# Kernel optimization log

Hardware: AMD Instinct MI355X
Metric: run time of the kernel (lower is better)

Reference implementation:

```python
import jax, jax.numpy as jnp
from jax import lax
import numpy as np

N = 2000      # num_nodes
T_IN = 24
T_OUT = 12
B = 32
H = 64        # hidden_dim
D = 10        # embed_dim / adapt_dim
K = 2         # cheb_k
C_IN = 1


def setup_inputs() -> dict:
    key = jax.random.key(0)
    ks = jax.random.split(key, 13)
    s = 0.1  # xavier-ish scale
    f32 = jnp.float32
    return {
        "x": jax.random.normal(ks[0], (B, T_IN, N), f32),
        "node_emb": jax.random.normal(ks[1], (N, D), f32) * s,
        "adapt_emb": jax.random.normal(ks[2], (N, D), f32) * s,
        # layer 0 NAPL weight/bias pools (gate: 2H out, candidate: H out)
        "Wg0": jax.random.normal(ks[3], (D, K, C_IN + H, 2 * H), f32) * s,
        "bg0": jax.random.normal(ks[4], (D, 2 * H), f32) * s,
        "Wc0": jax.random.normal(ks[5], (D, K, C_IN + H, H), f32) * s,
        "bc0": jax.random.normal(ks[6], (D, H), f32) * s,
        # layer 1 pools (input is hidden_dim)
        "Wg1": jax.random.normal(ks[7], (D, K, 2 * H, 2 * H), f32) * s,
        "bg1": jax.random.normal(ks[8], (D, 2 * H), f32) * s,
        "Wc1": jax.random.normal(ks[9], (D, K, 2 * H, H), f32) * s,
        "bc1": jax.random.normal(ks[10], (D, H), f32) * s,
        # 1x1 conv head == per-node linear hidden -> T_out
        "head_w": jax.random.normal(ks[11], (T_OUT, H), f32) * s,
        "head_b": jnp.zeros((T_OUT,), f32),
    }


def reference(x, node_emb, adapt_emb, Wg0, bg0, Wc0, bc0, Wg1, bg1, Wc1, bc1,
              head_w, head_b):
    Bn, T, Nn = x.shape
    # adaptive adjacency: row-softmax(relu(E E^T)); no prior -> A_used = A_adapt
    A = jax.nn.softmax(jax.nn.relu(adapt_emb @ adapt_emb.T), axis=-1)
    supports = jnp.stack([jnp.eye(Nn, dtype=x.dtype), A])  # (K, N, N)

    def napl(Wp, bp):
        # node-adaptive parameter learning: per-node weights/biases
        W = jnp.einsum('nd,dkio->nkio', node_emb, Wp)  # (N, K, Cin, Cout)
        b = node_emb @ bp                              # (N, Cout)
        return W, b

    p = [napl(Wg0, bg0), napl(Wc0, bc0), napl(Wg1, bg1), napl(Wc1, bc1)]

    def gconv(inp, W, b):
        # inp: (B, N, C)
        xg = jnp.einsum('knm,bmc->bknc', supports, inp)      # (B, K, N, C)
        return jnp.einsum('bkni,nkio->bno', xg, W) + b       # (B, N, Cout)

    def cell(xt, h, gW, gb, cW, cb):
        zr = jax.nn.sigmoid(gconv(jnp.concatenate([xt, h], -1), gW, gb))
        z, r = jnp.split(zr, 2, axis=-1)
        hc = jnp.tanh(gconv(jnp.concatenate([xt, r * h], -1), cW, cb))
        return z * h + (1.0 - z) * hc

    def step(carry, xt):
        h0, h1 = carry
        h0 = cell(xt, h0, p[0][0], p[0][1], p[1][0], p[1][1])
        h1 = cell(h0, h1, p[2][0], p[2][1], p[3][0], p[3][1])
        return (h0, h1), None

    xs = jnp.transpose(x[..., None], (1, 0, 2, 3))  # (T, B, N, 1)
    h0 = jnp.zeros((Bn, Nn, H), x.dtype)
    h1 = jnp.zeros((Bn, Nn, H), x.dtype)
    (h0, h1), _ = lax.scan(step, (h0, h1), xs)

    # 1x1 conv head on (B, H, N, 1) == per-node linear: (B, T_out, N)
    y = jnp.einsum('bnh,oh->bon', h1, head_w) + head_b[None, :, None]
    return y
```

## Files before the change

kernel.cpp:

```cpp
#include <hip/hip_runtime.h>
#include <math.h>

#define NN 2000
#define BB 32
#define TT 24
#define T_OUT 12
#define HH 64
#define DD 10
#define NP 2048
#define BC 2048

typedef unsigned short ushort_t;
typedef __bf16 bf16x8 __attribute__((ext_vector_type(8)));
typedef float f32x4 __attribute__((ext_vector_type(4)));

__device__ __forceinline__ float sigmoidf_(float x) { return 1.f / (1.f + expf(-x)); }

__device__ __forceinline__ ushort_t f2bf(float f) {
    unsigned int u = __float_as_uint(f);
    unsigned int r = (u + 0x7FFFu + ((u >> 16) & 1u)) >> 16;
    return (ushort_t)r;
}
__device__ __forceinline__ float bf2f(ushort_t s) {
    return __uint_as_float(((unsigned int)s) << 16);
}

__device__ __forceinline__ void glld16(const ushort_t* g, ushort_t* lds) {
    __builtin_amdgcn_global_load_lds(
        (const __attribute__((address_space(1))) char*)g,
        (__attribute__((address_space(3))) char*)lds, 16, 0, 0);
}

__device__ __forceinline__ unsigned lds_off(const void* p) {
    return (unsigned)(size_t)(__attribute__((address_space(3))) const char*)p;
}

constexpr size_t SZ_NPNP2 = (size_t)NP * NP * 2;
constexpr size_t SZ_ST4   = (size_t)NN * BC * 4;
constexpr size_t SZ_NPB2  = (size_t)NP * BC * 2;

constexpr size_t ABF_OFF  = 0;
constexpr size_t H0F_OFF  = ABF_OFF + SZ_NPNP2;
constexpr size_t H1F_OFF  = H0F_OFF + SZ_ST4;
constexpr size_t ZF_OFF   = H1F_OFF + SZ_ST4;
constexpr size_t H0B_OFF  = ZF_OFF + SZ_ST4;
constexpr size_t H1B_OFF  = H0B_OFF + SZ_NPB2;
constexpr size_t RHB_OFF  = H1B_OFF + SZ_NPB2;
constexpr size_t AH0_OFF  = RHB_OFF + SZ_NPB2;
constexpr size_t AHX_OFF  = AH0_OFF + SZ_NPB2;
constexpr size_t AXF_OFF  = AHX_OFF + SZ_NPB2;
constexpr size_t BTG0_OFF = AXF_OFF + (size_t)BB * TT * NN * 4;
constexpr size_t BTC0_OFF = BTG0_OFF + (size_t)DD * 128 * 128 * 2;
constexpr size_t BTG1_OFF = BTC0_OFF + (size_t)DD * 64 * 128 * 2;
constexpr size_t BTC1_OFF = BTG1_OFF + (size_t)DD * 128 * 256 * 2;
constexpr size_t WS_TOP   = BTC1_OFF + (size_t)DD * 64 * 256 * 2;
constexpr size_t ZF1_OFF  = WS_TOP;
constexpr size_t RHB1_OFF = ZF1_OFF + SZ_ST4;
constexpr size_t AHY_OFF  = RHB1_OFF + SZ_NPB2;
constexpr size_t TOP_PIPE = AHY_OFF + SZ_NPB2;

__global__ __launch_bounds__(256) void compute_A_kernel(const float* __restrict__ E,
                                                        float* __restrict__ A) {
    const int row = blockIdx.x;
    const int tid = threadIdx.x;
    float er[DD];
#pragma unroll
    for (int d = 0; d < DD; ++d) er[d] = E[row * DD + d];
    __shared__ float red[8];

    float lmax = -1e30f;
    for (int c = tid; c < NN; c += 256) {
        float s = 0.f;
#pragma unroll
        for (int d = 0; d < DD; ++d) s += er[d] * E[c * DD + d];
        s = fmaxf(s, 0.f);
        A[(size_t)row * NN + c] = s;
        lmax = fmaxf(lmax, s);
    }
#pragma unroll
    for (int o = 32; o > 0; o >>= 1) lmax = fmaxf(lmax, __shfl_down(lmax, o, 64));
    if ((tid & 63) == 0) red[tid >> 6] = lmax;
    __syncthreads();
    const float rmax = fmaxf(fmaxf(red[0], red[1]), fmaxf(red[2], red[3]));
    __syncthreads();

    float lsum = 0.f;
    for (int c = tid; c < NN; c += 256) {
        float v = expf(A[(size_t)row * NN + c] - rmax);
        A[(size_t)row * NN + c] = v;
        lsum += v;
    }
#pragma unroll
    for (int o = 32; o > 0; o >>= 1) lsum += __shfl_down(lsum, o, 64);
    if ((tid & 63) == 0) red[4 + (tid >> 6)] = lsum;
    __syncthreads();
    const float inv = 1.f / (red[4] + red[5] + red[6] + red[7]);
    for (int c = tid; c < NN; c += 256) A[(size_t)row * NN + c] *= inv;
}

__global__ __launch_bounds__(256) void convert_A(const float* __restrict__ Af,
                                                 ushort_t* __restrict__ Ab) {
    size_t idx = (size_t)blockIdx.x * 256 + threadIdx.x;
    int r = (int)(idx >> 11), c = (int)(idx & 2047);
    float v = (r < NN && c < NN) ? Af[(size_t)r * NN + c] : 0.f;
    Ab[idx] = f2bf(v);
}

__global__ __launch_bounds__(256) void ax2_kernel(const float* __restrict__ A,
                                                  const float* __restrict__ x,
                                                  float* __restrict__ Ax) {
    __shared__ float As[64][66];
    __shared__ float xs[64][50];
    const int n0 = blockIdx.x * 64;
    const int b0 = blockIdx.y * 2;
    const int tid = threadIdx.x;
    const int tr = tid >> 4, tc = tid & 15;
    float acc[4][3] = {};

    for (int m0 = 0; m0 < NN; m0 += 64) {
#pragma unroll
        for (int l = 0; l < 16; ++l) {
            int idx = tid + l * 256;
            int mm = idx & 63, r = idx >> 6;
            int n = n0 + r, m = m0 + mm;
            As[mm][r] = (n < NN && m < NN) ? A[(size_t)n * NN + m] : 0.f;
        }
#pragma unroll
        for (int l = 0; l < 12; ++l) {
            int idx = tid + l * 256;
            int mm = idx & 63, col = idx >> 6;
            int m = m0 + mm;
            int bl = col / 24, t = col - bl * 24;
            xs[mm][col] = (m < NN) ? x[((size_t)(b0 + bl) * TT + t) * NN + m] : 0.f;
        }
        __syncthreads();
#pragma unroll 4
        for (int mm = 0; mm < 64; ++mm) {
            float2 a01 = *(const float2*)&As[mm][tr * 4];
            float2 a23 = *(const float2*)&As[mm][tr * 4 + 2];
            float xv[3];
            xv[0] = xs[mm][tc * 3];
            xv[1] = xs[mm][tc * 3 + 1];
            xv[2] = xs[mm][tc * 3 + 2];
            float av[4] = {a01.x, a01.y, a23.x, a23.y};
#pragma unroll
            for (int i = 0; i < 4; ++i)
#pragma unroll
                for (int j = 0; j < 3; ++j) acc[i][j] += av[i] * xv[j];
        }
        __syncthreads();
    }
#pragma unroll
    for (int i = 0; i < 4; ++i) {
        const int n = n0 + tr * 4 + i;
        if (n < NN) {
#pragma unroll
            for (int j = 0; j < 3; ++j) {
                int col = tc * 3 + j;
                int bl = col / 24, t = col - bl * 24;
                Ax[((size_t)(b0 + bl) * TT + t) * NN + n] = acc[i][j];
            }
        }
    }
}


__device__ __forceinline__ void gemm_body(int bx, int by,
                                          const ushort_t* __restrict__ Ab,
                                          const ushort_t* __restrict__ H,
                                          ushort_t* __restrict__ Y, char* smem) {
    ushort_t* As = (ushort_t*)smem;
    ushort_t* Bs = (ushort_t*)(smem + 8192);
    const int tid = threadIdx.x;
    const int w = tid >> 6, l = tid & 63, lr = l & 15, lg = l >> 4;
    const int n0 = bx * 64, j0 = by * 128;
    f32x4 acc[4][2] = {};

    const unsigned bs0 = lds_off(Bs);
    const unsigned btr_b[2] = {
        bs0 + 2u * ((unsigned)(w * 2 + 0) * 512 + (unsigned)lg * 128 + (unsigned)lr),
        bs0 + 2u * ((unsigned)(w * 2 + 1) * 512 + (unsigned)lg * 128 + (unsigned)lr)};

    for (int ks = 0; ks < NP / 64; ++ks) {
        const int k0 = ks * 64;
#pragma unroll
        for (int p = 0; p < 2; ++p) {
            const int idx = p * 256 + tid;
            const int row = idx >> 3, sl = idx & 7;
            glld16(Ab + (size_t)(n0 + row) * NP + k0 + ((sl ^ (row & 7)) << 3),
                   (ushort_t*)((char*)As + idx * 16));
        }
#pragma unroll
        for (int p = 0; p < 4; ++p) {
            const int idx = p * 256 + tid;
            const int g = idx >> 9, li = idx & 511;
            const int row = k0 + g * 32 + ((li >> 3) & 7) * 4 + ((li >> 1) & 3);
            const int col = j0 + (li >> 6) * 16 + (li & 1) * 8;
            glld16(H + (size_t)row * BC + col,
                   (ushort_t*)((char*)Bs + g * 8192 + li * 16));
        }
        __syncthreads();

        bf16x8 av[2][4];
#pragma unroll
        for (int kk = 0; kk < 2; ++kk)
#pragma unroll
            for (int m = 0; m < 4; ++m) {
                const int rr = m * 16 + lr;
                av[kk][m] = *(const bf16x8*)&As[rr * 64 + (((kk * 4 + lg) ^ (rr & 7)) << 3)];
            }
        unsigned long long bq[2][2][2];
        asm volatile(
            "ds_read_b64_tr_b16 %0, %8 offset:0\n\t"
            "ds_read_b64_tr_b16 %1, %8 offset:128\n\t"
            "ds_read_b64_tr_b16 %2, %9 offset:0\n\t"
            "ds_read_b64_tr_b16 %3, %9 offset:128\n\t"
            "ds_read_b64_tr_b16 %4, %8 offset:8192\n\t"
            "ds_read_b64_tr_b16 %5, %8 offset:8320\n\t"
            "ds_read_b64_tr_b16 %6, %9 offset:8192\n\t"
            "ds_read_b64_tr_b16 %7, %9 offset:8320"
            : "=v"(bq[0][0][0]), "=v"(bq[0][0][1]), "=v"(bq[0][1][0]), "=v"(bq[0][1][1]),
              "=v"(bq[1][0][0]), "=v"(bq[1][0][1]), "=v"(bq[1][1][0]), "=v"(bq[1][1][1])
            : "v"(btr_b[0]), "v"(btr_b[1]));
        asm volatile("s_waitcnt lgkmcnt(0)" ::: "memory");
        __builtin_amdgcn_sched_barrier(0);
        bf16x8 bv[2][2];
#pragma unroll
        for (int kk = 0; kk < 2; ++kk)
#pragma unroll
            for (int nt = 0; nt < 2; ++nt) {
                union { unsigned long long q[2]; bf16x8 f; } u;
                u.q[0] = bq[kk][nt][0];
                u.q[1] = bq[kk][nt][1];
                bv[kk][nt] = u.f;
            }

#pragma unroll
        for (int kk = 0; kk < 2; ++kk)
#pragma unroll
            for (int m = 0; m < 4; ++m)
#pragma unroll
                for (int nt = 0; nt < 2; ++nt)
                    acc[m][nt] = __builtin_amdgcn_mfma_f32_16x16x32_bf16(av[kk][m], bv[kk][nt], acc[m][nt], 0, 0, 0);
        __syncthreads();
    }

#pragma unroll
    for (int m = 0; m < 4; ++m)
#pragma unroll
        for (int r = 0; r < 4; ++r) {
            const int n = n0 + m * 16 + lg * 4 + r;
            if (n < NN) {
#pragma unroll
                for (int nt = 0; nt < 2; ++nt)
                    Y[(size_t)n * BC + j0 + w * 32 + nt * 16 + lr] = f2bf(acc[m][nt][r]);
            }
        }
}

template <int NSEGS, int CO, bool GATE, bool HASX>
__device__ __forceinline__ void napl_body(
    int bid, char* smem,
    const ushort_t* __restrict__ Bt, const float* __restrict__ bp,
    const float* __restrict__ emb, const float* __restrict__ WxPool,
    const ushort_t* __restrict__ s0p, const ushort_t* __restrict__ s1p,
    const ushort_t* __restrict__ s2p, const ushort_t* __restrict__ s3p,
    const float* __restrict__ xv, const float* __restrict__ axv,
    const float* hf, float* __restrict__ zf,
    ushort_t* __restrict__ outb, float* outf, int t) {
    constexpr int K = NSEGS * 64;
    constexpr int NT = (CO == 128) ? 2 : 1;
    constexpr int NHALF = NSEGS / 2;
    ushort_t* As = (ushort_t*)smem;
    const int tid = threadIdx.x;
    const int w = tid >> 6, l = tid & 63, lr = l & 15, lg = l >> 4;
    const int n0 = bid * 2;
    const int ob = w * (16 * NT);
    const ushort_t* segs[4] = {s0p, s1p, s2p, s3p};

#pragma unroll
    for (int s = 0; s < NSEGS; ++s) {
        const ushort_t* sp = segs[s];
#pragma unroll
        for (int p = 0; p < 2; ++p) {
            const int idx = p * 256 + tid;
            const int row = idx >> 3, c16 = idx & 7;
            glld16(sp + (size_t)(n0 + (row >> 5)) * BC + (row & 31) * 64 +
                       ((c16 ^ (row & 7)) << 3),
                   (ushort_t*)((char*)As + s * 8192 + idx * 16));
        }
    }
    __syncthreads();

    f32x4 OUT[4][NT] = {};
#pragma unroll 1
    for (int hf2 = 0; hf2 < NHALF; ++hf2) {
        bf16x8 av[4][4];
#pragma unroll
        for (int c = 0; c < 4; ++c) {
            const int s = hf2 * 2 + (c >> 1);
            const int kin = (c & 1) * 32 + lg * 8;
#pragma unroll
            for (int m = 0; m < 4; ++m) {
                const int rr = m * 16 + lr;
                av[c][m] = *(const bf16x8*)&As[s * 4096 + rr * 64 + (kin ^ ((rr & 7) << 3))];
            }
        }
#pragma unroll 1
        for (int d = 0; d < DD; ++d) {
            const ushort_t* btd = Bt + (size_t)d * CO * K;
            const float ea = emb[n0 * DD + d];
            const float eb = emb[(n0 + 1) * DD + d];
            f32x4 P[4][NT] = {};
#pragma unroll
            for (int c = 0; c < 4; ++c) {
                const int kg = (hf2 * 2 + (c >> 1)) * 64 + (c & 1) * 32 + lg * 8;
                bf16x8 bv[NT];
#pragma unroll
                for (int nt = 0; nt < NT; ++nt)
                    bv[nt] = *(const bf16x8*)&btd[(size_t)(ob + nt * 16 + lr) * K + kg];
#pragma unroll
                for (int m = 0; m < 4; ++m)
#pragma unroll
                    for (int nt = 0; nt < NT; ++nt)
                        P[m][nt] = __builtin_amdgcn_mfma_f32_16x16x32_bf16(av[c][m], bv[nt], P[m][nt], 0, 0, 0);
            }
#pragma unroll
            for (int m = 0; m < 4; ++m) {
                const float e = (m < 2) ? ea : eb;
#pragma unroll
                for (int nt = 0; nt < NT; ++nt)
#pragma unroll
                    for (int r = 0; r < 4; ++r)
                        OUT[m][nt][r] += e * P[m][nt][r];
            }
        }
    }

    float bias[2][NT];
#pragma unroll
    for (int nd = 0; nd < 2; ++nd)
#pragma unroll
        for (int nt = 0; nt < NT; ++nt) {
            float s_ = 0.f;
#pragma unroll
            for (int d = 0; d < DD; ++d)
                s_ += emb[(n0 + nd) * DD + d] * bp[d * CO + ob + nt * 16 + lr];
            bias[nd][nt] = s_;
        }
    float wx[2][2][NT] = {};
    if (HASX) {
#pragma unroll
        for (int kk = 0; kk < 2; ++kk)
#pragma unroll
            for (int nd = 0; nd < 2; ++nd)
#pragma unroll
                for (int nt = 0; nt < NT; ++nt) {
                    float s_ = 0.f;
#pragma unroll
                    for (int d = 0; d < DD; ++d)
                        s_ += emb[(n0 + nd) * DD + d] *
                              WxPool[(size_t)(d * 2 + kk) * 65 * CO + ob + nt * 16 + lr];
                    wx[kk][nd][nt] = s_;
                }
    }

#pragma unroll
    for (int m = 0; m < 4; ++m) {
        const int nd = m >> 1;
        const int n = n0 + nd;
#pragma unroll
        for (int r = 0; r < 4; ++r) {
            const int row = m * 16 + lg * 4 + r;
            const int b = row & 31;
            const size_t nb = (size_t)n * BC + b * 64;
            float xt = 0.f, axt = 0.f;
            if (HASX) {
                xt = xv[((size_t)b * TT + t) * NN + n];
                axt = axv[((size_t)b * TT + t) * NN + n];
            }
#pragma unroll
            for (int nt = 0; nt < NT; ++nt) {
                const int o = ob + nt * 16 + lr;
                float val = OUT[m][nt][r] + bias[nd][nt];
                if (HASX) val += xt * wx[0][nd][nt] + axt * wx[1][nd][nt];
                if (GATE) {
                    const float sg = sigmoidf_(val);
                    if (ob < 64) {
                        zf[nb + o] = sg;
                    } else {
                        outb[nb + (o - 64)] = f2bf(sg * hf[nb + (o - 64)]);
                    }
                } else {
                    const float hc = tanhf(val);
                    const float z = zf[nb + o];
                    const float hn = z * hf[nb + o] + (1.f - z) * hc;
                    outf[nb + o] = hn;
                    outb[nb + o] = f2bf(hn);
                }
            }
        }
    }
}


__global__ __launch_bounds__(256) void gemm_trb(const ushort_t* __restrict__ Ab,
                                                const ushort_t* __restrict__ H0,
                                                ushort_t* __restrict__ Y0,
                                                const ushort_t* __restrict__ H1,
                                                ushort_t* __restrict__ Y1) {
    __shared__ __align__(16) char smem[24576];
    gemm_body(blockIdx.x, blockIdx.y, Ab,
              (blockIdx.z == 0) ? H0 : H1, (blockIdx.z == 0) ? Y0 : Y1, smem);
}

template <int NSEGS, int CO, bool GATE, bool HASX>
__global__ __launch_bounds__(256) void napl2(
    const ushort_t* __restrict__ Bt, const float* __restrict__ bp,
    const float* __restrict__ emb, const float* __restrict__ WxPool,
    const ushort_t* __restrict__ s0p, const ushort_t* __restrict__ s1p,
    const ushort_t* __restrict__ s2p, const ushort_t* __restrict__ s3p,
    const float* __restrict__ xv, const float* __restrict__ axv,
    const float* hf, float* __restrict__ zf,
    ushort_t* __restrict__ outb, float* outf, int t) {
    __shared__ __align__(16) char smem[NSEGS * 8192];
    napl_body<NSEGS, CO, GATE, HASX>(blockIdx.x, smem, Bt, bp, emb, WxPool,
                                     s0p, s1p, s2p, s3p, xv, axv, hf, zf, outb, outf, t);
}

__global__ __launch_bounds__(256) void mergeA_k(
    const ushort_t* __restrict__ Abf, const ushort_t* __restrict__ Hg,
    ushort_t* __restrict__ Yg,
    const ushort_t* __restrict__ Bt, const float* __restrict__ bp,
    const float* __restrict__ emb, const float* __restrict__ Wx,
    const ushort_t* __restrict__ s0, const ushort_t* __restrict__ s1,
    const float* __restrict__ xv, const float* __restrict__ axv,
    const float* hf, float* __restrict__ zf, ushort_t* __restrict__ outb, int t) {
    __shared__ __align__(16) char smem[24576];
    const int g = blockIdx.x;
    if (g < 512)
        gemm_body(g & 31, g >> 5, Abf, Hg, Yg, smem);
    else
        napl_body<2, 128, true, true>(g - 512, smem, Bt, bp, emb, Wx,
                                      s0, s1, s0, s0, xv, axv, hf, zf, outb, nullptr, t);
}

__global__ __launch_bounds__(256) void mergeB_k(
    const ushort_t* __restrict__ Abf, const ushort_t* __restrict__ Hg,
    ushort_t* __restrict__ Yg,
    const ushort_t* __restrict__ Bt, const float* __restrict__ bp,
    const float* __restrict__ emb,
    const ushort_t* __restrict__ s0, const ushort_t* __restrict__ s1,
    const ushort_t* __restrict__ s2, const ushort_t* __restrict__ s3,
    const float* hf, float* __restrict__ zf,
    ushort_t* __restrict__ outb, float* outf, int t) {
    __shared__ __align__(16) char smem[32768];
    const int g = blockIdx.x;
    if (g < 512)
        gemm_body(g & 31, g >> 5, Abf, Hg, Yg, smem);
    else
        napl_body<4, 64, false, false>(g - 512, smem, Bt, bp, emb, nullptr,
                                       s0, s1, s2, s3, nullptr, nullptr, hf, zf, outb, outf, t);
}

__global__ __launch_bounds__(256) void mergeC_k(
    const ushort_t* __restrict__ Abf, const ushort_t* __restrict__ Hg,
    ushort_t* __restrict__ Yg,
    const ushort_t* __restrict__ Bt, const float* __restrict__ bp,
    const float* __restrict__ emb, const float* __restrict__ Wx,
    const ushort_t* __restrict__ s0, const ushort_t* __restrict__ s1,
    const float* __restrict__ xv, const float* __restrict__ axv,
    const float* hf, float* __restrict__ zf,
    ushort_t* __restrict__ outb, float* outf, int t) {
    __shared__ __align__(16) char smem[24576];
    const int g = blockIdx.x;
    if (g < 512)
        gemm_body(g & 31, g >> 5, Abf, Hg, Yg, smem);
    else
        napl_body<2, 64, false, true>(g - 512, smem, Bt, bp, emb, Wx,
                                      s0, s1, s0, s0, xv, axv, hf, zf, outb, outf, t);
}

template <int CI, int CO, bool L0>
__global__ __launch_bounds__(256) void prepW(const float* __restrict__ Wp,
                                             ushort_t* __restrict__ Bt) {
    constexpr int K = L0 ? 128 : 256;
    const int idx = blockIdx.x * 256 + threadIdx.x;
    if (idx >= DD * CO * K) return;
    const int d = idx / (CO * K);
    const int rem = idx - d * CO * K;
    const int o = rem / K;
    const int k = rem - o * K;
    const int s = k >> 6, c = k & 63;
    const int kk = L0 ? s : (s & 1);
    const int i = L0 ? (1 + c) : ((s >> 1) * 64 + c);
    Bt[idx] = f2bf(Wp[((size_t)(d * 2 + kk) * CI + i) * CO + o]);
}

__global__ __launch_bounds__(256) void head_kernel(const float* __restrict__ h1,
                                                   const float* __restrict__ hw,
                                                   const float* __restrict__ hb,
                                                   float* __restrict__ y) {
    __shared__ float wl[T_OUT * HH];
    const int tid = threadIdx.x;
    for (int idx = tid; idx < T_OUT * HH; idx += 256) wl[idx] = hw[idx];
    __syncthreads();
    const int gi = blockIdx.x * 256 + tid;
    if (gi >= BB * NN) return;
    const int b = gi / NN, n = gi % NN;
    float acc[T_OUT];
#pragma unroll
    for (int ot = 0; ot < T_OUT; ++ot) acc[ot] = hb[ot];
    for (int h = 0; h < HH; ++h) {
        float v = h1[(size_t)n * BC + b * 64 + h];
#pragma unroll
        for (int ot = 0; ot < T_OUT; ++ot) acc[ot] += v * wl[ot * HH + h];
    }
#pragma unroll
    for (int ot = 0; ot < T_OUT; ++ot)
        y[((size_t)b * T_OUT + ot) * NN + n] = acc[ot];
}

extern "C" void kernel_launch(void* const* d_in, const int* in_sizes, int n_in,
                              void* d_out, int out_size, void* d_ws, size_t ws_size,
                              hipStream_t stream) {
    const float* x = (const float*)d_in[0];
    const float* node_emb = (const float*)d_in[1];
    const float* adapt_emb = (const float*)d_in[2];
    const float* Wg0 = (const float*)d_in[3];
    const float* bg0 = (const float*)d_in[4];
    const float* Wc0 = (const float*)d_in[5];
    const float* bc0 = (const float*)d_in[6];
    const float* Wg1 = (const float*)d_in[7];
    const float* bg1 = (const float*)d_in[8];
    const float* Wc1 = (const float*)d_in[9];
    const float* bc1 = (const float*)d_in[10];
    const float* head_w = (const float*)d_in[11];
    const float* head_b = (const float*)d_in[12];
    float* y = (float*)d_out;

    char* ws = (char*)d_ws;
    ushort_t* Abf  = (ushort_t*)(ws + ABF_OFF);
    float* h0f = (float*)(ws + H0F_OFF);
    float* h1f = (float*)(ws + H1F_OFF);
    float* zf  = (float*)(ws + ZF_OFF);
    ushort_t* h0b = (ushort_t*)(ws + H0B_OFF);
    ushort_t* h1b = (ushort_t*)(ws + H1B_OFF);
    ushort_t* rhb = (ushort_t*)(ws + RHB_OFF);
    ushort_t* Ah0 = (ushort_t*)(ws + AH0_OFF);
    ushort_t* AhX = (ushort_t*)(ws + AHX_OFF);
    float* Axf = (float*)(ws + AXF_OFF);
    ushort_t* Btg0 = (ushort_t*)(ws + BTG0_OFF);
    ushort_t* Btc0 = (ushort_t*)(ws + BTC0_OFF);
    ushort_t* Btg1 = (ushort_t*)(ws + BTG1_OFF);
    ushort_t* Btc1 = (ushort_t*)(ws + BTC1_OFF);
    float* Af32 = zf;

    const bool pipe = (ws_size >= TOP_PIPE);

    hipMemsetAsync(h0f, 0, SZ_ST4, stream);
    hipMemsetAsync(h1f, 0, SZ_ST4, stream);
    hipMemsetAsync(h0b, 0, SZ_NPB2, stream);
    hipMemsetAsync(h1b, 0, SZ_NPB2, stream);
    hipMemsetAsync(rhb, 0, SZ_NPB2, stream);
    hipMemsetAsync(Ah0, 0, SZ_NPB2, stream);
    hipMemsetAsync(AhX, 0, SZ_NPB2, stream);

    compute_A_kernel<<<NN, 256, 0, stream>>>(adapt_emb, Af32);
    ax2_kernel<<<dim3(32, 16), 256, 0, stream>>>(Af32, x, Axf);
    convert_A<<<(NP * NP) / 256, 256, 0, stream>>>(Af32, Abf);
    prepW<65, 128, true><<<(DD * 128 * 128 + 255) / 256, 256, 0, stream>>>(Wg0, Btg0);
    prepW<65, 64, true><<<(DD * 64 * 128 + 255) / 256, 256, 0, stream>>>(Wc0, Btc0);
    prepW<128, 128, false><<<(DD * 128 * 256 + 255) / 256, 256, 0, stream>>>(Wg1, Btg1);
    prepW<128, 64, false><<<(DD * 64 * 256 + 255) / 256, 256, 0, stream>>>(Wc1, Btc1);

    const dim3 gG1(NP / 64, NP / 128, 1);
    const dim3 gG2(NP / 64, NP / 128, 2);
    const int gN = NN * BB / 64;

    if (pipe) {
        float* zf0 = zf;
        ushort_t* rhb0 = rhb;
        float* zf1 = (float*)(ws + ZF1_OFF);
        ushort_t* rhb1 = (ushort_t*)(ws + RHB1_OFF);
        ushort_t* AhY = (ushort_t*)(ws + AHY_OFF);
        hipMemsetAsync(rhb1, 0, SZ_NPB2, stream);

        napl2<2, 128, true, true><<<gN, 256, 0, stream>>>(
            Btg0, bg0, node_emb, Wg0, h0b, Ah0, h0b, h0b, x, Axf, h0f, zf0, rhb0, nullptr, 0);
        gemm_trb<<<gG1, 256, 0, stream>>>(Abf, rhb0, AhY, rhb0, AhY);
        napl2<2, 64, false, true><<<gN, 256, 0, stream>>>(
            Btc0, bc0, node_emb, Wc0, rhb0, AhY, rhb0, rhb0, x, Axf, h0f, zf0, h0b, h0f, 0);
        gemm_trb<<<gG2, 256, 0, stream>>>(Abf, h0b, Ah0, h1b, AhX);
        napl2<4, 128, true, false><<<gN, 256, 0, stream>>>(
            Btg1, bg1, node_emb, nullptr, h0b, Ah0, h1b, AhX, nullptr, nullptr, h1f, zf1, rhb1, nullptr, 0);

        for (int t = 0; t < TT - 1; ++t) {
            mergeA_k<<<1512, 256, 0, stream>>>(Abf, rhb1, AhX,
                Btg0, bg0, node_emb, Wg0, h0b, Ah0, x, Axf, h0f, zf0, rhb0, t + 1);
            mergeB_k<<<1512, 256, 0, stream>>>(Abf, rhb0, AhY,
                Btc1, bc1, node_emb, h0b, Ah0, rhb1, AhX, h1f, zf1, h1b, h1f, t);
            mergeC_k<<<1512, 256, 0, stream>>>(Abf, h1b, AhX,
                Btc0, bc0, node_emb, Wc0, rhb0, AhY, x, Axf, h0f, zf0, h0b, h0f, t + 1);
            gemm_trb<<<gG1, 256, 0, stream>>>(Abf, h0b, Ah0, h0b, Ah0);
            napl2<4, 128, true, false><<<gN, 256, 0, stream>>>(
                Btg1, bg1, node_emb, nullptr, h0b, Ah0, h1b, AhX, nullptr, nullptr, h1f, zf1, rhb1, nullptr, t + 1);
        }
        gemm_trb<<<gG1, 256, 0, stream>>>(Abf, rhb1, AhX, rhb1, AhX);
        napl2<4, 64, false, false><<<gN, 256, 0, stream>>>(
            Btc1, bc1, node_emb, nullptr, h0b, Ah0, rhb1, AhX, nullptr, nullptr, h1f, zf1, h1b, h1f, TT - 1);
    } else {
        for (int t = 0; t < TT; ++t) {
            napl2<2, 128, true, true><<<gN, 256, 0, stream>>>(
                Btg0, bg0, node_emb, Wg0, h0b, Ah0, h0b, h0b, x, Axf, h0f, zf, rhb, nullptr, t);
            gemm_trb<<<gG1, 256, 0, stream>>>(Abf, rhb, AhX, rhb, AhX);
            napl2<2, 64, false, true><<<gN, 256, 0, stream>>>(
                Btc0, bc0, node_emb, Wc0, rhb, AhX, rhb, rhb, x, Axf, h0f, zf, h0b, h0f, t);
            gemm_trb<<<gG2, 256, 0, stream>>>(Abf, h0b, Ah0, h1b, AhX);
            napl2<4, 128, true, false><<<gN, 256, 0, stream>>>(
                Btg1, bg1, node_emb, nullptr, h0b, Ah0, h1b, AhX, nullptr, nullptr, h1f, zf, rhb, nullptr, t);
            gemm_trb<<<gG1, 256, 0, stream>>>(Abf, rhb, AhX, rhb, AhX);
            napl2<4, 64, false, false><<<gN, 256, 0, stream>>>(
                Btc1, bc1, node_emb, nullptr, h0b, Ah0, rhb, AhX, nullptr, nullptr, h1f, zf, h1b, h1f, t);
        }
    }

    head_kernel<<<(BB * NN + 255) / 256, 256, 0, stream>>>(h1f, head_w, head_b, y);
}
```

Before: 8.671 ms.

## Skew layer-0 step t+1 with layer-1 step t into merged NAPL launches

```diff
diff --git a/kernel.cpp b/kernel.cpp
--- a/kernel.cpp
+++ b/kernel.cpp
@@ -58,6 +58,8 @@
 constexpr size_t RHB1_OFF = ZF1_OFF + SZ_ST4;
 constexpr size_t AHY_OFF  = RHB1_OFF + SZ_NPB2;
 constexpr size_t TOP_PIPE = AHY_OFF + SZ_NPB2;
+constexpr size_t H0B2_OFF = TOP_PIPE;
+constexpr size_t TOP_PIPE2 = H0B2_OFF + SZ_NPB2;
 
 __global__ __launch_bounds__(256) void compute_A_kernel(const float* __restrict__ E,
                                                         float* __restrict__ A) {
@@ -481,6 +483,52 @@
                                       s0, s1, s0, s0, xv, axv, hf, zf, outb, outf, t);
 }
 
+__global__ __launch_bounds__(256) void mergeG_k(
+    const ushort_t* __restrict__ Btg1, const float* __restrict__ bg1,
+    const ushort_t* __restrict__ Btg0, const float* __restrict__ bg0,
+    const float* __restrict__ emb, const float* __restrict__ Wg0,
+    const ushort_t* __restrict__ hbt, const ushort_t* __restrict__ Ah0,
+    const ushort_t* __restrict__ h1b, const ushort_t* __restrict__ AhX,
+    const float* __restrict__ xv, const float* __restrict__ axv,
+    const float* h0f, const float* h1f,
+    float* __restrict__ zf0, float* __restrict__ zf1,
+    ushort_t* __restrict__ rhb0, ushort_t* __restrict__ rhb1, int t) {
+    __shared__ __align__(16) char smem[32768];
+    const int g = blockIdx.x;
+    if (g < 1000)
+        napl_body<4, 128, true, false>(g, smem, Btg1, bg1, emb, nullptr,
+                                       hbt, Ah0, h1b, AhX, nullptr, nullptr,
+                                       h1f, zf1, rhb1, nullptr, t);
+    else
+        napl_body<2, 128, true, true>(g - 1000, smem, Btg0, bg0, emb, Wg0,
+                                      hbt, Ah0, hbt, hbt, xv, axv,
+                                      h0f, zf0, rhb0, nullptr, t + 1);
+}
+
+__global__ __launch_bounds__(256) void mergeCC_k(
+    const ushort_t* __restrict__ Btc1, const float* __restrict__ bc1,
+    const ushort_t* __restrict__ Btc0, const float* __restrict__ bc0,
+    const float* __restrict__ emb, const float* __restrict__ Wc0,
+    const ushort_t* __restrict__ hbt, ushort_t* __restrict__ hbt1,
+    const ushort_t* __restrict__ Ah0, const ushort_t* __restrict__ rhb1,
+    const ushort_t* __restrict__ AhX, const ushort_t* __restrict__ AhY,
+    const ushort_t* __restrict__ rhb0,
+    const float* __restrict__ xv, const float* __restrict__ axv,
+    float* h0f, float* h1f,
+    float* __restrict__ zf0, float* __restrict__ zf1,
+    ushort_t* __restrict__ h1b, int t) {
+    __shared__ __align__(16) char smem[32768];
+    const int g = blockIdx.x;
+    if (g < 1000)
+        napl_body<4, 64, false, false>(g, smem, Btc1, bc1, emb, nullptr,
+                                       hbt, Ah0, rhb1, AhX, nullptr, nullptr,
+                                       h1f, zf1, h1b, h1f, t);
+    else
+        napl_body<2, 64, false, true>(g - 1000, smem, Btc0, bc0, emb, Wc0,
+                                      rhb0, AhY, rhb0, rhb0, xv, axv,
+                                      h0f, zf0, hbt1, h0f, t + 1);
+}
+
 template <int CI, int CO, bool L0>
 __global__ __launch_bounds__(256) void prepW(const float* __restrict__ Wp,
                                              ushort_t* __restrict__ Bt) {
@@ -556,6 +604,7 @@
     ushort_t* Btc1 = (ushort_t*)(ws + BTC1_OFF);
     float* Af32 = zf;
 
+    const bool pipe2 = (ws_size >= TOP_PIPE2);
     const bool pipe = (ws_size >= TOP_PIPE);
 
     hipMemsetAsync(h0f, 0, SZ_ST4, stream);
@@ -578,7 +627,43 @@
     const dim3 gG2(NP / 64, NP / 128, 2);
     const int gN = NN * BB / 64;
 
-    if (pipe) {
+    if (pipe2) {
+        float* zf0 = zf;
+        ushort_t* rhb0 = rhb;
+        float* zf1 = (float*)(ws + ZF1_OFF);
+        ushort_t* rhb1 = (ushort_t*)(ws + RHB1_OFF);
+        ushort_t* AhY = (ushort_t*)(ws + AHY_OFF);
+        ushort_t* h0b2 = (ushort_t*)(ws + H0B2_OFF);
+        hipMemsetAsync(rhb1, 0, SZ_NPB2, stream);
+        hipMemsetAsync(h0b2, 0, SZ_NPB2, stream);
+        ushort_t* hb[2] = {h0b, h0b2};
+
+        napl2<2, 128, true, true><<<gN, 256, 0, stream>>>(
+            Btg0, bg0, node_emb, Wg0, h0b, Ah0, h0b, h0b, x, Axf, h0f, zf0, rhb0, nullptr, 0);
+        gemm_trb<<<gG1, 256, 0, stream>>>(Abf, rhb0, AhY, rhb0, AhY);
+        napl2<2, 64, false, true><<<gN, 256, 0, stream>>>(
+            Btc0, bc0, node_emb, Wc0, rhb0, AhY, rhb0, rhb0, x, Axf, h0f, zf0, hb[0], h0f, 0);
+        gemm_trb<<<gG1, 256, 0, stream>>>(Abf, hb[0], Ah0, hb[0], Ah0);
+
+        for (int t = 0; t < TT - 1; ++t) {
+            ushort_t* hbt = hb[t & 1];
+            ushort_t* hbt1 = hb[(t + 1) & 1];
+            mergeG_k<<<2000, 256, 0, stream>>>(Btg1, bg1, Btg0, bg0, node_emb, Wg0,
+                hbt, Ah0, h1b, AhX, x, Axf, h0f, h1f, zf0, zf1, rhb0, rhb1, t);
+            gemm_trb<<<gG2, 256, 0, stream>>>(Abf, rhb1, AhX, rhb0, AhY);
+            mergeCC_k<<<2000, 256, 0, stream>>>(Btc1, bc1, Btc0, bc0, node_emb, Wc0,
+                hbt, hbt1, Ah0, rhb1, AhX, AhY, rhb0, x, Axf, h0f, h1f, zf0, zf1, h1b, t);
+            gemm_trb<<<gG2, 256, 0, stream>>>(Abf, h1b, AhX, hbt1, Ah0);
+        }
+        {
+            ushort_t* hbT = hb[(TT - 1) & 1];
+            napl2<4, 128, true, false><<<gN, 256, 0, stream>>>(
+                Btg1, bg1, node_emb, nullptr, hbT, Ah0, h1b, AhX, nullptr, nullptr, h1f, zf1, rhb1, nullptr, TT - 1);
+            gemm_trb<<<gG1, 256, 0, stream>>>(Abf, rhb1, AhX, rhb1, AhX);
+            napl2<4, 64, false, false><<<gN, 256, 0, stream>>>(
+                Btc1, bc1, node_emb, nullptr, hbT, Ah0, rhb1, AhX, nullptr, nullptr, h1f, zf1, h1b, h1f, TT - 1);
+        }
+    } else if (pipe) {
         float* zf0 = zf;
         ushort_t* rhb0 = rhb;
         float* zf1 = (float*)(ws + ZF1_OFF);
```

Measured after the change: 8.601 ms. Within noise of the previous version (-0.8%).
